# Optimization experiments

Measured on AMD Instinct MI355X. Metric: run time of the kernel, lower is better.

The kernel has to match this reference:

```python
import jax, jax.numpy as jnp
import numpy as np

C_IN, C_OUT, K, PAD, STRIDE = 128, 256, 3, 1, 1
H = W = 256


def setup_inputs() -> dict:
    key = jax.random.key(0)
    k1, k2, k3 = jax.random.split(key, 3)
    # batch=1: the original forward uses X_pad[0] for every batch index,
    # so with m=1 the buggy loop and a standard conv are mathematically identical.
    x = jax.random.normal(k1, (1, C_IN, H, W), dtype=jnp.float32)
    # nn.Parameter(torch.rand(...)) -> uniform[0,1)
    weight = jax.random.uniform(k2, (C_OUT, C_IN, K, K), dtype=jnp.float32)
    bias = jax.random.uniform(k3, (C_OUT,), dtype=jnp.float32)
    return {"x": x, "weight": weight, "bias": bias}


def reference(x, weight, bias):
    # Faithful math of convAppx.forward with FP_appx_mul treated as exact
    # multiply (FP_appx_mul is not defined in the source): a plain 2D
    # cross-correlation (no kernel flip, matching the sliced elementwise
    # product) with symmetric padding, stride 1, plus per-channel bias.
    z = jax.lax.conv_general_dilated(
        x, weight,
        window_strides=(STRIDE, STRIDE),
        padding=((PAD, PAD), (PAD, PAD)),
        dimension_numbers=("NCHW", "OIHW", "NCHW"),
    )
    return z + bias[None, :, None, None]
```

## Files before the change

### kernel.cpp

```cpp
#include <hip/hip_runtime.h>
#include <hip/hip_bf16.h>


typedef short bf16x8 __attribute__((ext_vector_type(8)));
typedef float f32x4 __attribute__((ext_vector_type(4)));
typedef unsigned short u16x4 __attribute__((ext_vector_type(4)));
typedef unsigned short u16x8 __attribute__((ext_vector_type(8)));

#define CIN   128
#define COUT  256
#define HH    256
#define WW    256
#define HP    258
#define ROWP  (HP * CIN)

static __device__ __forceinline__ unsigned short f2bf(float v) {
    __hip_bfloat16 b = __float2bfloat16(v);
    return *reinterpret_cast<unsigned short*>(&b);
}

static __device__ __forceinline__ void gload_lds16(const unsigned short* g, unsigned short* l) {
    __builtin_amdgcn_global_load_lds(
        (const __attribute__((address_space(1))) unsigned int*)g,
        (__attribute__((address_space(3))) unsigned int*)l, 16, 0, 0);
}

__global__ __launch_bounds__(256) void prep_kernel(const float* __restrict__ x,
                                                   const float* __restrict__ w,
                                                   unsigned short* __restrict__ xb,
                                                   unsigned short* __restrict__ wr) {
    int bid = blockIdx.x;
    int t   = threadIdx.x;

    if (bid < 65) {
        int i = bid * 256 + t;
        if (i < 16448) {
            u16x8 z = {0, 0, 0, 0, 0, 0, 0, 0};
            int off;
            if (i < 8256) {
                int r   = (i >= 4128) ? 1 : 0;
                int rem = i - r * 4128;
                off = (r * 257) * ROWP + rem * 8;
            } else {
                int j   = i - 8256;
                int col = j >> 12;
                int rem = j & 4095;
                int hp  = (rem >> 4) + 1;
                int c8  = rem & 15;
                off = hp * ROWP + (col * 257) * CIN + c8 * 8;
            }
            *(u16x8*)(&xb[off]) = z;
        }
    }

    if (bid < 128) {
        int p = bid * 256 + t;
        const float* src = w + p * 9;
        #pragma unroll
        for (int khw = 0; khw < 9; ++khw)
            wr[khw * (COUT * CIN) + p] = f2bf(src[khw]);
    }

    int h  = bid >> 2;
    int w0 = (bid & 3) * 64;
    __shared__ unsigned short tile[CIN * 72];

    int wq  = t & 15;
    int cib = t >> 4;
    for (int c0 = 0; c0 < CIN; c0 += 16) {
        int ci = c0 + cib;
        float4 v = *(const float4*)(x + ci * (HH * WW) + h * WW + w0 + wq * 4);
        u16x4 p;
        p.x = f2bf(v.x); p.y = f2bf(v.y); p.z = f2bf(v.z); p.w = f2bf(v.w);
        *(u16x4*)(&tile[ci * 72 + wq * 4]) = p;
    }
    __syncthreads();

    for (int it = 0; it < 4; ++it) {
        int idx = it * 256 + t;
        int ww_ = idx & 63;
        int c8  = idx >> 6;
        u16x8 o;
        #pragma unroll
        for (int j = 0; j < 8; ++j)
            o[j] = tile[(c8 * 8 + j) * 72 + ww_];
        int dst = ((h + 1) * HP + (w0 + ww_ + 1)) * CIN + c8 * 8;
        *(u16x8*)(&xb[dst]) = o;
    }
}

__global__ __launch_bounds__(512, 2) void conv_mfma_kernel(const unsigned short* __restrict__ xb,
                                                           const unsigned short* __restrict__ wr,
                                                           const float* __restrict__ bias,
                                                           float* __restrict__ out) {
    __shared__ unsigned short Bw[258 * 128];
    __shared__ unsigned short As[256 * 128];

    int bid = blockIdx.x;
    int h   = (bid & 7) * 32 + (bid >> 3);

    int t    = threadIdx.x;
    int wave = t >> 6;
    int lane = t & 63;
    int wm   = wave >> 1;
    int wn   = wave & 1;
    int quad = lane >> 4;
    int l16  = lane & 15;

    f32x4 acc[4][8];
    #pragma unroll
    for (int mi = 0; mi < 4; ++mi)
        #pragma unroll
        for (int ni = 0; ni < 8; ++ni)
            acc[mi][ni] = (f32x4){0.f, 0.f, 0.f, 0.f};

    for (int kh = 0; kh < 3; ++kh) {
        const unsigned short* xrow = xb + (size_t)(h + kh) * ROWP;
        for (int kw = 0; kw < 3; ++kw) {
            int khw = kh * 3 + kw;
            __syncthreads();
            if (kw == 0) {
                #pragma unroll
                for (int it = 0; it < 8; ++it) {
                    int seg = it * 512 + t;
                    int col = seg >> 4;
                    int s   = seg & 15;
                    int c   = s ^ (col & 15);
                    gload_lds16(xrow + col * CIN + c * 8, &Bw[seg * 8]);
                }
                if (t < 32) {
                    int seg = 4096 + t;
                    int col = seg >> 4;
                    int s   = seg & 15;
                    int c   = s ^ (col & 15);
                    gload_lds16(xrow + col * CIN + c * 8, &Bw[seg * 8]);
                }
            }
            {
                const unsigned short* wsrc = wr + (size_t)khw * (COUT * CIN);
                #pragma unroll
                for (int it = 0; it < 8; ++it) {
                    int seg = it * 512 + t;
                    int r   = seg >> 4;
                    int s   = seg & 15;
                    int c   = s ^ (r & 15);
                    gload_lds16(wsrc + r * CIN + c * 8, &As[seg * 8]);
                }
            }
            __syncthreads();
            #pragma unroll
            for (int kk = 0; kk < 4; ++kk) {
                int chunk = kk * 4 + quad;
                bf16x8 af[4], bfr[8];
                #pragma unroll
                for (int mi = 0; mi < 4; ++mi) {
                    int row = wm * 64 + mi * 16 + l16;
                    af[mi] = *(bf16x8*)(&As[row * 128 + (chunk ^ l16) * 8]);
                }
                #pragma unroll
                for (int ni = 0; ni < 8; ++ni) {
                    int col = wn * 128 + ni * 16 + l16 + kw;
                    bfr[ni] = *(bf16x8*)(&Bw[col * 128 + (chunk ^ (col & 15)) * 8]);
                }
                #pragma unroll
                for (int mi = 0; mi < 4; ++mi)
                    #pragma unroll
                    for (int ni = 0; ni < 8; ++ni)
                        acc[mi][ni] = __builtin_amdgcn_mfma_f32_16x16x32_bf16(
                            af[mi], bfr[ni], acc[mi][ni], 0, 0, 0);
            }
        }
    }

    int sp0 = wn * 128 + l16;
    #pragma unroll
    for (int mi = 0; mi < 4; ++mi) {
        #pragma unroll
        for (int r = 0; r < 4; ++r) {
            int co = wm * 64 + mi * 16 + quad * 4 + r;
            float b = bias[co];
            float* orow = out + (size_t)co * (HH * WW) + h * WW + sp0;
            #pragma unroll
            for (int ni = 0; ni < 8; ++ni)
                orow[ni * 16] = acc[mi][ni][r] + b;
        }
    }
}

extern "C" void kernel_launch(void* const* d_in, const int* in_sizes, int n_in,
                              void* d_out, int out_size, void* d_ws, size_t ws_size,
                              hipStream_t stream) {
    const float* x    = (const float*)d_in[0];
    const float* w    = (const float*)d_in[1];
    const float* bias = (const float*)d_in[2];
    float* out        = (float*)d_out;

    unsigned short* xb = (unsigned short*)d_ws;
    unsigned short* wr = xb + (size_t)HP * HP * CIN;

    prep_kernel<<<dim3(1024), dim3(256), 0, stream>>>(x, w, xb, wr);
    conv_mfma_kernel<<<dim3(256), dim3(512), 0, stream>>>(xb, wr, bias, out);
}
```

Baseline: 134.1 us.

## Double-buffer half-channel weight tiles to overlap loads with MFMA compute

Splits each 3x3 tap's weight tile into two 64-channel halves and double-buffers them in LDS. The next half is prefetched with global_load_lds while the current one feeds the MFMAs, using a partial vmcnt wait instead of a full syncthreads, plus setprio around the compute. The goal is to hide the weight-load latency that was previously serialized between barriers on each of the nine taps. The cost is twice as many barrier rounds per block, hand-written waitcnt logic that must be exactly right, and one wasted prefetch on the final iteration.

```diff
diff --git a/kernel.cpp b/kernel.cpp
--- a/kernel.cpp
+++ b/kernel.cpp
@@ -94,14 +94,14 @@
                                                            const float* __restrict__ bias,
                                                            float* __restrict__ out) {
     __shared__ unsigned short Bw[258 * 128];
-    __shared__ unsigned short As[256 * 128];
+    __shared__ unsigned short Ah[2][256 * 64];
 
     int bid = blockIdx.x;
     int h   = (bid & 7) * 32 + (bid >> 3);
 
     int t    = threadIdx.x;
+    int lane = t & 63;
     int wave = t >> 6;
-    int lane = t & 63;
     int wm   = wave >> 1;
     int wn   = wave & 1;
     int quad = lane >> 4;
@@ -114,62 +114,82 @@
         for (int ni = 0; ni < 8; ++ni)
             acc[mi][ni] = (f32x4){0.f, 0.f, 0.f, 0.f};
 
-    for (int kh = 0; kh < 3; ++kh) {
-        const unsigned short* xrow = xb + (size_t)(h + kh) * ROWP;
-        for (int kw = 0; kw < 3; ++kw) {
-            int khw = kh * 3 + kw;
-            __syncthreads();
-            if (kw == 0) {
+    auto stageA = [&](int idx, unsigned short* dst) {
+        int khw_  = idx >> 1;
+        int half_ = idx & 1;
+        const unsigned short* wsrc = wr + (size_t)khw_ * (COUT * CIN) + half_ * 64;
+        #pragma unroll
+        for (int it = 0; it < 4; ++it) {
+            int seg = it * 512 + t;
+            int r   = seg >> 3;
+            int s   = seg & 7;
+            int c   = s ^ (r & 7);
+            gload_lds16(wsrc + r * CIN + c * 8, &dst[seg * 8]);
+        }
+    };
+
+    stageA(0, Ah[0]);
+
+    for (int i = 0; i < 18; ++i) {
+        int khw  = i >> 1;
+        int half = i & 1;
+        int kw   = khw % 3;
+
+        if ((i % 6) == 0) {
+            const unsigned short* xrow = xb + (size_t)(h + i / 6) * ROWP;
+            #pragma unroll
+            for (int it = 0; it < 8; ++it) {
+                int seg = it * 512 + t;
+                int col = seg >> 4;
+                int s   = seg & 15;
+                int c   = s ^ (col & 15);
+                gload_lds16(xrow + col * CIN + c * 8, &Bw[seg * 8]);
+            }
+            if (t < 32) {
+                int seg = 4096 + t;
+                int col = seg >> 4;
+                int s   = seg & 15;
+                int c   = s ^ (col & 15);
+                gload_lds16(xrow + col * CIN + c * 8, &Bw[seg * 8]);
+            }
+        }
+
+        int nxt = (i + 1) % 18;
+        stageA(nxt, Ah[nxt & 1]);
+
+        asm volatile("s_waitcnt vmcnt(4)" ::: "memory");
+        __builtin_amdgcn_s_barrier();
+        __builtin_amdgcn_sched_barrier(0);
+
+        const unsigned short* Acur = Ah[i & 1];
+        __builtin_amdgcn_s_setprio(1);
+        #pragma unroll
+        for (int kkk = 0; kkk < 2; ++kkk) {
+            int lc = kkk * 4 + quad;
+            int cg = half * 8 + lc;
+            bf16x8 af[4], bfr[8];
+            #pragma unroll
+            for (int mi = 0; mi < 4; ++mi) {
+                int row = wm * 64 + mi * 16 + l16;
+                af[mi] = *(bf16x8*)(&Acur[row * 64 + (lc ^ (l16 & 7)) * 8]);
+            }
+            #pragma unroll
+            for (int ni = 0; ni < 8; ++ni) {
+                int col = wn * 128 + ni * 16 + l16 + kw;
+                bfr[ni] = *(bf16x8*)(&Bw[col * 128 + (cg ^ (col & 15)) * 8]);
+            }
+            #pragma unroll
+            for (int mi = 0; mi < 4; ++mi)
                 #pragma unroll
-                for (int it = 0; it < 8; ++it) {
-                    int seg = it * 512 + t;
-                    int col = seg >> 4;
-                    int s   = seg & 15;
-                    int c   = s ^ (col & 15);
-                    gload_lds16(xrow + col * CIN + c * 8, &Bw[seg * 8]);
-                }
-                if (t < 32) {
-                    int seg = 4096 + t;
-                    int col = seg >> 4;
-                    int s   = seg & 15;
-                    int c   = s ^ (col & 15);
-                    gload_lds16(xrow + col * CIN + c * 8, &Bw[seg * 8]);
-                }
-            }
-            {
-                const unsigned short* wsrc = wr + (size_t)khw * (COUT * CIN);
-                #pragma unroll
-                for (int it = 0; it < 8; ++it) {
-                    int seg = it * 512 + t;
-                    int r   = seg >> 4;
-                    int s   = seg & 15;
-                    int c   = s ^ (r & 15);
-                    gload_lds16(wsrc + r * CIN + c * 8, &As[seg * 8]);
-                }
-            }
-            __syncthreads();
-            #pragma unroll
-            for (int kk = 0; kk < 4; ++kk) {
-                int chunk = kk * 4 + quad;
-                bf16x8 af[4], bfr[8];
-                #pragma unroll
-                for (int mi = 0; mi < 4; ++mi) {
-                    int row = wm * 64 + mi * 16 + l16;
-                    af[mi] = *(bf16x8*)(&As[row * 128 + (chunk ^ l16) * 8]);
-                }
-                #pragma unroll
-                for (int ni = 0; ni < 8; ++ni) {
-                    int col = wn * 128 + ni * 16 + l16 + kw;
-                    bfr[ni] = *(bf16x8*)(&Bw[col * 128 + (chunk ^ (col & 15)) * 8]);
-                }
-                #pragma unroll
-                for (int mi = 0; mi < 4; ++mi)
-                    #pragma unroll
-                    for (int ni = 0; ni < 8; ++ni)
-                        acc[mi][ni] = __builtin_amdgcn_mfma_f32_16x16x32_bf16(
-                            af[mi], bfr[ni], acc[mi][ni], 0, 0, 0);
-            }
-        }
+                for (int ni = 0; ni < 8; ++ni)
+                    acc[mi][ni] = __builtin_amdgcn_mfma_f32_16x16x32_bf16(
+                        af[mi], bfr[ni], acc[mi][ni], 0, 0, 0);
+        }
+        __builtin_amdgcn_s_setprio(0);
+
+        asm volatile("s_waitcnt lgkmcnt(0)" ::: "memory");
+        __builtin_amdgcn_s_barrier();
+        __builtin_amdgcn_sched_barrier(0);
     }
 
     int sp0 = wn * 128 + l16;
```

New measurement: 136.2 us. Within noise of the previous version (+1.6%).
